# Optimization experiments

Measured on AMD Instinct MI355X. Metric: run time of the kernel, lower is better.

## Reference

```python
import jax, jax.numpy as jnp
import numpy as np

B, H = 16384, 1024
EPS = 1e-5


def setup_inputs() -> dict:
    key = jax.random.key(0)
    ks = jax.random.split(key, 12)
    inp = {
        "t": 0,
        "h": jax.random.normal(ks[0], (B, H), jnp.float32),
        "e": jax.random.normal(ks[1], (B, H), jnp.float32),
        # LiquidNeuron params
        "W_rec": jax.random.normal(ks[2], (H, H), jnp.float32) * 0.1,
        "bias": jnp.zeros((H,), jnp.float32),
        "tau": jnp.ones((H,), jnp.float32),
        "decay": jnp.ones((H,), jnp.float32),
        "ln_w": jnp.ones((H,), jnp.float32),
        "ln_b": jnp.zeros((H,), jnp.float32),
        # context_encoder: Linear -> ReLU -> Linear (dropout = identity in eval)
        "ce_w1": jax.random.normal(ks[3], (H, H), jnp.float32) * (1.0 / np.sqrt(H)),
        "ce_b1": jnp.zeros((H,), jnp.float32),
        "ce_w2": jax.random.normal(ks[4], (H, H), jnp.float32) * (1.0 / np.sqrt(H)),
        "ce_b2": jnp.zeros((H,), jnp.float32),
        # param_modulator
        "pm_w": jax.random.normal(ks[5], (H, H), jnp.float32) * (1.0 / np.sqrt(H)),
        "pm_b": jnp.zeros((H,), jnp.float32),
    }
    return inp


def reference(t, h, e, W_rec, bias, tau, decay, ln_w, ln_b,
              ce_w1, ce_b1, ce_w2, ce_b2, pm_w, pm_b):
    # context encoder (eval mode: dropout is identity)
    context = jnp.maximum(h @ ce_w1.T + ce_b1, 0.0) @ ce_w2.T + ce_b2  # [B,H]
    pa = context @ pm_w.T + pm_b  # param_adjustment [B,H]
    # bmm(e[:,None,:], (W_rec*(1+pa)[:,:,None]).T) == (1+pa) * (e @ W_rec.T)
    matmul_result = (1.0 + pa) * (e @ W_rec.T)  # [B,H]
    tau_adjusted = tau * jax.nn.sigmoid(pa)  # [B,H]
    dh_dt = (-decay * h + matmul_result + bias) / tau_adjusted
    # LayerNorm over last dim
    mu = jnp.mean(dh_dt, axis=-1, keepdims=True)
    var = jnp.var(dh_dt, axis=-1, keepdims=True)
    dh_dt = (dh_dt - mu) * jax.lax.rsqrt(var + EPS) * ln_w + ln_b
    return dh_dt
```

## Files before the change

kernel.cpp:

```cpp
#include <hip/hip_runtime.h>
#include <stdint.h>

#define H_DIM 1024
#define B_DIM 16384

typedef unsigned short u16;
typedef short bf16x8 __attribute__((ext_vector_type(8)));
typedef float f32x4 __attribute__((ext_vector_type(4)));

__device__ __forceinline__ u16 f2bf(float f) {
  union { float f; uint32_t u; } v; v.f = f;
  uint32_t r = v.u + 0x7fffu + ((v.u >> 16) & 1u);
  return (u16)(r >> 16);
}

#define GLDS16(gsrc, ldst)                                                                 \
  __builtin_amdgcn_global_load_lds((const __attribute__((address_space(1))) void*)(gsrc),  \
                                   (__attribute__((address_space(3))) void*)(ldst), 16, 0, 0)

__global__ __launch_bounds__(256) void cvt_f32_bf16(const float* __restrict__ in,
                                                    u16* __restrict__ out, int n4) {
  int i = blockIdx.x * blockDim.x + threadIdx.x;
  const int stride = gridDim.x * blockDim.x;
  const float4* __restrict__ in4 = (const float4*)in;
  ushort4* __restrict__ out4 = (ushort4*)out;
  for (; i < n4; i += stride) {
    float4 v = in4[i];
    ushort4 o;
    o.x = f2bf(v.x); o.y = f2bf(v.y); o.z = f2bf(v.z); o.w = f2bf(v.w);
    out4[i] = o;
  }
}

__global__ __launch_bounds__(256) void cvt4_f32_bf16(const float* __restrict__ a0,
                                                     const float* __restrict__ a1,
                                                     const float* __restrict__ a2,
                                                     const float* __restrict__ a3,
                                                     u16* __restrict__ o0, u16* __restrict__ o1,
                                                     u16* __restrict__ o2, u16* __restrict__ o3) {
  const int which = blockIdx.x >> 8;
  const float* in = which == 0 ? a0 : which == 1 ? a1 : which == 2 ? a2 : a3;
  u16* out = which == 0 ? o0 : which == 1 ? o1 : which == 2 ? o2 : o3;
  const int n4 = (H_DIM * H_DIM) / 4;
  int i = (blockIdx.x & 255) * 256 + threadIdx.x;
  const float4* in4 = (const float4*)in;
  ushort4* out4 = (ushort4*)out;
  for (; i < n4; i += 256 * 256) {
    float4 v = in4[i];
    ushort4 o;
    o.x = f2bf(v.x); o.y = f2bf(v.y); o.z = f2bf(v.z); o.w = f2bf(v.w);
    out4[i] = o;
  }
}


template <int MODE>
__device__ __forceinline__ void subtile_step(u16* shp, int slot, int slot3, int aoff, int boff,
                                             int wv, const u16*& pA0, const u16*& pA1,
                                             const u16*& pB0, const u16*& pB1,
                                             f32x4 (&acc)[8][4]) {
  const u16* Ab = shp + slot * 16384 + aoff;
  const u16* Bb = shp + slot * 16384 + 8192 + boff;
  bf16x8 aF[8], bF[4];
#pragma unroll
  for (int i = 0; i < 4; ++i) aF[i] = *(const bf16x8*)(Ab + i * 512);
#pragma unroll
  for (int i = 0; i < 4; ++i) bF[i] = *(const bf16x8*)(Bb + i * 512);
#pragma unroll
  for (int i = 4; i < 8; ++i) aF[i] = *(const bf16x8*)(Ab + i * 512);
  if (MODE == 3) {
    u16* da = shp + slot3 * 16384 + wv * 1024;
    GLDS16(pA0, da); GLDS16(pA1, da + 512);
    u16* db = shp + slot3 * 16384 + 8192 + wv * 1024;
    GLDS16(pB0, db); GLDS16(pB1, db + 512);
    pA0 += 32; pA1 += 32; pB0 += 32; pB1 += 32;
  }
  __builtin_amdgcn_s_barrier();
  __builtin_amdgcn_s_setprio(1);
#pragma unroll
  for (int mf = 0; mf < 4; ++mf)
#pragma unroll
    for (int nf = 0; nf < 4; ++nf)
      acc[mf][nf] = __builtin_amdgcn_mfma_f32_16x16x32_bf16(aF[mf], bF[nf], acc[mf][nf], 0, 0, 0);
#pragma unroll
  for (int mf = 4; mf < 8; ++mf)
#pragma unroll
    for (int nf = 0; nf < 4; ++nf)
      acc[mf][nf] = __builtin_amdgcn_mfma_f32_16x16x32_bf16(aF[mf], bF[nf], acc[mf][nf], 0, 0, 0);
  __builtin_amdgcn_s_setprio(0);
  if (MODE == 3) asm volatile("s_waitcnt vmcnt(8)" ::: "memory");
  if (MODE == 2) asm volatile("s_waitcnt vmcnt(4)" ::: "memory");
  if (MODE == 1) asm volatile("s_waitcnt vmcnt(0)" ::: "memory");
  __builtin_amdgcn_s_barrier();
}

template <bool RELU, bool HASBIAS, typename OUT>
__global__ __launch_bounds__(512, 2) void gemm256(const u16* __restrict__ A,
                                                  const u16* __restrict__ W,
                                                  const float* __restrict__ bias,
                                                  OUT* __restrict__ C) {
  extern __shared__ u16 sh[];
  const int t = threadIdx.x;
  const int wv = t >> 6, l = t & 63;
  const int wm = wv >> 2, wn = wv & 3;
  const int l15 = l & 15, lg = l >> 4;

  const int bid = blockIdx.x;
  const int logical = (bid & 7) * 32 + (bid >> 3);
  const int m0 = (logical >> 2) * 256;
  const int n0 = (logical & 3) * 256;

  const int koff = (lg ^ ((l15 >> 1) & 3)) * 8;
  const int aoff = (wm * 128 + l15) * 32 + koff;
  const int boff = (wn * 64 + l15) * 32 + koff;

  const int rowst = wv * 32 + (l >> 2);
  const int ksl = ((l & 3) ^ ((l >> 3) & 3)) * 8;
  const u16* pA0 = A + (size_t)(m0 + rowst) * H_DIM + ksl;
  const u16* pA1 = pA0 + 16 * H_DIM;
  const u16* pB0 = W + (size_t)(n0 + rowst) * H_DIM + ksl;
  const u16* pB1 = pB0 + 16 * H_DIM;

  f32x4 acc[8][4] = {};

#pragma unroll
  for (int s = 0; s < 3; ++s) {
    u16* da = sh + s * 16384 + wv * 1024;
    GLDS16(pA0, da); GLDS16(pA1, da + 512);
    u16* db = sh + s * 16384 + 8192 + wv * 1024;
    GLDS16(pB0, db); GLDS16(pB1, db + 512);
    pA0 += 32; pA1 += 32; pB0 += 32; pB1 += 32;
  }
  asm volatile("s_waitcnt vmcnt(8)" ::: "memory");
  __builtin_amdgcn_s_barrier();

  for (int s = 0; s < 29; ++s)
    subtile_step<3>(sh, s & 3, (s + 3) & 3, aoff, boff, wv, pA0, pA1, pB0, pB1, acc);
  subtile_step<2>(sh, 1, 0, aoff, boff, wv, pA0, pA1, pB0, pB1, acc);
  subtile_step<1>(sh, 2, 0, aoff, boff, wv, pA0, pA1, pB0, pB1, acc);
  subtile_step<0>(sh, 3, 0, aoff, boff, wv, pA0, pA1, pB0, pB1, acc);

  float bv[4];
#pragma unroll
  for (int nf = 0; nf < 4; ++nf)
    bv[nf] = HASBIAS ? bias[n0 + wn * 64 + nf * 16 + l15] : 0.0f;
#pragma unroll
  for (int mf = 0; mf < 8; ++mf) {
#pragma unroll
    for (int nf = 0; nf < 4; ++nf) {
      const int col = n0 + wn * 64 + nf * 16 + l15;
#pragma unroll
      for (int j = 0; j < 4; ++j) {
        const int row = m0 + wm * 128 + mf * 16 + lg * 4 + j;
        float v = acc[mf][nf][j] + bv[nf];
        if (RELU) v = fmaxf(v, 0.0f);
        if constexpr (sizeof(OUT) == 2)
          C[(size_t)row * H_DIM + col] = (OUT)f2bf(v);
        else
          C[(size_t)row * H_DIM + col] = v;
      }
    }
  }
}

__global__ __launch_bounds__(256) void liquid_ln(const float* __restrict__ h,
                                                 const float* __restrict__ pa,
                                                 const float* __restrict__ ev,
                                                 const float* __restrict__ bias,
                                                 const float* __restrict__ tau,
                                                 const float* __restrict__ decay,
                                                 const float* __restrict__ lnw,
                                                 const float* __restrict__ lnb,
                                                 float* __restrict__ out) {
  const int wv = threadIdx.x >> 6, l = threadIdx.x & 63;
  const int row = blockIdx.x * 4 + wv;
  const size_t base = (size_t)row * H_DIM + l * 16;
  const int pc = l * 16;

  float d[16];
  float s = 0.f, ss = 0.f;
#pragma unroll
  for (int c = 0; c < 4; ++c) {
    float hf[4], pf[4], ef[4], bf_[4], tf[4], df[4];
    *(float4*)hf = *(const float4*)(h + base + c * 4);
    *(float4*)pf = *(const float4*)(pa + base + c * 4);
    *(float4*)ef = *(const float4*)(ev + base + c * 4);
    *(float4*)bf_ = *(const float4*)(bias + pc + c * 4);
    *(float4*)tf = *(const float4*)(tau + pc + c * 4);
    *(float4*)df = *(const float4*)(decay + pc + c * 4);
#pragma unroll
    for (int j = 0; j < 4; ++j) {
      const float sig = 1.0f / (1.0f + __expf(-pf[j]));
      const float num = fmaf(-df[j], hf[j], fmaf(1.0f + pf[j], ef[j], bf_[j]));
      const float val = num / (tf[j] * sig);
      d[c * 4 + j] = val;
      s += val;
      ss += val * val;
    }
  }
#pragma unroll
  for (int off = 32; off; off >>= 1) {
    s += __shfl_xor(s, off);
    ss += __shfl_xor(ss, off);
  }
  const float mu = s * (1.0f / H_DIM);
  const float var = ss * (1.0f / H_DIM) - mu * mu;
  const float rstd = rsqrtf(var + 1e-5f);

#pragma unroll
  for (int c = 0; c < 4; ++c) {
    float lw[4], lb[4], o[4];
    *(float4*)lw = *(const float4*)(lnw + pc + c * 4);
    *(float4*)lb = *(const float4*)(lnb + pc + c * 4);
#pragma unroll
    for (int j = 0; j < 4; ++j) o[j] = fmaf((d[c * 4 + j] - mu) * rstd, lw[j], lb[j]);
    *(float4*)(out + base + c * 4) = *(float4*)o;
  }
}

extern "C" void kernel_launch(void* const* d_in, const int* in_sizes, int n_in,
                              void* d_out, int out_size, void* d_ws, size_t ws_size,
                              hipStream_t stream) {
  const float* h = (const float*)d_in[1];
  const float* e = (const float*)d_in[2];
  const float* Wrec = (const float*)d_in[3];
  const float* bias = (const float*)d_in[4];
  const float* tau = (const float*)d_in[5];
  const float* decay = (const float*)d_in[6];
  const float* lnw = (const float*)d_in[7];
  const float* lnb = (const float*)d_in[8];
  const float* ce_w1 = (const float*)d_in[9];
  const float* ce_b1 = (const float*)d_in[10];
  const float* ce_w2 = (const float*)d_in[11];
  const float* ce_b2 = (const float*)d_in[12];
  const float* pm_w = (const float*)d_in[13];
  const float* pm_b = (const float*)d_in[14];
  float* out = (float*)d_out;

  char* ws = (char*)d_ws;
  const size_t MB = 1024 * 1024;
  u16* w1b = (u16*)(ws + 0 * MB);
  u16* w2b = (u16*)(ws + 2 * MB);
  u16* w3b = (u16*)(ws + 4 * MB);
  u16* w4b = (u16*)(ws + 6 * MB);
  u16* ebf = (u16*)(ws + 8 * MB);
  u16* hbf = (u16*)(ws + 40 * MB);
  u16* t1 = (u16*)(ws + 72 * MB);
  u16* ctx = (u16*)(ws + 104 * MB);
  float* paf = (float*)(ws + 40 * MB);
  float* evf = (float*)(ws + 104 * MB);

  const int nBH4 = (B_DIM * H_DIM) / 4;
  cvt_f32_bf16<<<2048, 256, 0, stream>>>(h, hbf, nBH4);
  cvt_f32_bf16<<<2048, 256, 0, stream>>>(e, ebf, nBH4);
  cvt4_f32_bf16<<<1024, 256, 0, stream>>>(ce_w1, ce_w2, pm_w, Wrec, w1b, w2b, w3b, w4b);

  const int LDS_BYTES = 131072;
  hipFuncSetAttribute((const void*)gemm256<true, true, u16>,
                      hipFuncAttributeMaxDynamicSharedMemorySize, LDS_BYTES);
  hipFuncSetAttribute((const void*)gemm256<false, true, u16>,
                      hipFuncAttributeMaxDynamicSharedMemorySize, LDS_BYTES);
  hipFuncSetAttribute((const void*)gemm256<false, true, float>,
                      hipFuncAttributeMaxDynamicSharedMemorySize, LDS_BYTES);
  hipFuncSetAttribute((const void*)gemm256<false, false, float>,
                      hipFuncAttributeMaxDynamicSharedMemorySize, LDS_BYTES);

  const int NWG = (B_DIM / 256) * (H_DIM / 256);
  gemm256<true, true, u16><<<NWG, 512, LDS_BYTES, stream>>>(hbf, w1b, ce_b1, t1);
  gemm256<false, true, u16><<<NWG, 512, LDS_BYTES, stream>>>(t1, w2b, ce_b2, ctx);
  gemm256<false, true, float><<<NWG, 512, LDS_BYTES, stream>>>(ctx, w3b, pm_b, paf);
  gemm256<false, false, float><<<NWG, 512, LDS_BYTES, stream>>>(ebf, w4b, nullptr, evf);

  liquid_ln<<<B_DIM / 4, 256, 0, stream>>>(h, paf, evf, bias, tau, decay, lnw, lnb, out);
}
```

Before: 266.8 us.

## Store GEMM outputs in bf16, merge conversion kernels, precompute reciprocal tau, drop barrier

The last two GEMMs now write bf16 instead of fp32, which halves the intermediate writes and the reads of pa and e@W in the LayerNorm kernel. The two large activation conversions are merged into one launch, and 1/tau is precomputed in an extra block of the weight-conversion kernel. The LN kernel replaces its division with multiplies and uses 8-wide contiguous loads. One s_barrier between the LDS fragment reads and the MFMAs is removed, which may race with the async global-to-LDS prefetch. bf16 rounding of pa and ev adds error.

Measured after the change: 220.4 us. 1.21x faster.

```diff
diff --git a/kernel.cpp b/kernel.cpp
--- a/kernel.cpp
+++ b/kernel.cpp
@@ -6,6 +6,7 @@
 
 typedef unsigned short u16;
 typedef short bf16x8 __attribute__((ext_vector_type(8)));
+typedef unsigned short ushort8 __attribute__((ext_vector_type(8)));
 typedef float f32x4 __attribute__((ext_vector_type(4)));
 
 __device__ __forceinline__ u16 f2bf(float f) {
@@ -13,18 +14,27 @@
   uint32_t r = v.u + 0x7fffu + ((v.u >> 16) & 1u);
   return (u16)(r >> 16);
 }
+__device__ __forceinline__ float bf2f(u16 x) {
+  union { uint32_t u; float f; } v; v.u = ((uint32_t)x) << 16;
+  return v.f;
+}
 
 #define GLDS16(gsrc, ldst)                                                                 \
   __builtin_amdgcn_global_load_lds((const __attribute__((address_space(1))) void*)(gsrc),  \
                                    (__attribute__((address_space(3))) void*)(ldst), 16, 0, 0)
 
-__global__ __launch_bounds__(256) void cvt_f32_bf16(const float* __restrict__ in,
-                                                    u16* __restrict__ out, int n4) {
-  int i = blockIdx.x * blockDim.x + threadIdx.x;
-  const int stride = gridDim.x * blockDim.x;
-  const float4* __restrict__ in4 = (const float4*)in;
-  ushort4* __restrict__ out4 = (ushort4*)out;
-  for (; i < n4; i += stride) {
+__global__ __launch_bounds__(256) void cvt2_f32_bf16(const float* __restrict__ a0,
+                                                     const float* __restrict__ a1,
+                                                     u16* __restrict__ o0,
+                                                     u16* __restrict__ o1) {
+  const int which = blockIdx.x >> 11;
+  const float* in = which ? a1 : a0;
+  u16* out = which ? o1 : o0;
+  const int n4 = (B_DIM * H_DIM) / 4;
+  int i = (blockIdx.x & 2047) * 256 + threadIdx.x;
+  const float4* in4 = (const float4*)in;
+  ushort4* out4 = (ushort4*)out;
+  for (; i < n4; i += 2048 * 256) {
     float4 v = in4[i];
     ushort4 o;
     o.x = f2bf(v.x); o.y = f2bf(v.y); o.z = f2bf(v.z); o.w = f2bf(v.w);
@@ -37,7 +47,13 @@
                                                      const float* __restrict__ a2,
                                                      const float* __restrict__ a3,
                                                      u16* __restrict__ o0, u16* __restrict__ o1,
-                                                     u16* __restrict__ o2, u16* __restrict__ o3) {
+                                                     u16* __restrict__ o2, u16* __restrict__ o3,
+                                                     const float* __restrict__ tau,
+                                                     float* __restrict__ rtau) {
+  if (blockIdx.x >= 1024) {
+    for (int i = threadIdx.x; i < H_DIM; i += 256) rtau[i] = 1.0f / tau[i];
+    return;
+  }
   const int which = blockIdx.x >> 8;
   const float* in = which == 0 ? a0 : which == 1 ? a1 : which == 2 ? a2 : a3;
   u16* out = which == 0 ? o0 : which == 1 ? o1 : which == 2 ? o2 : o3;
@@ -75,7 +91,6 @@
     GLDS16(pB0, db); GLDS16(pB1, db + 512);
     pA0 += 32; pA1 += 32; pB0 += 32; pB1 += 32;
   }
-  __builtin_amdgcn_s_barrier();
   __builtin_amdgcn_s_setprio(1);
 #pragma unroll
   for (int mf = 0; mf < 4; ++mf)
@@ -164,36 +179,41 @@
 }
 
 __global__ __launch_bounds__(256) void liquid_ln(const float* __restrict__ h,
-                                                 const float* __restrict__ pa,
-                                                 const float* __restrict__ ev,
+                                                 const u16* __restrict__ pa,
+                                                 const u16* __restrict__ ev,
                                                  const float* __restrict__ bias,
-                                                 const float* __restrict__ tau,
+                                                 const float* __restrict__ rtau,
                                                  const float* __restrict__ decay,
                                                  const float* __restrict__ lnw,
                                                  const float* __restrict__ lnb,
                                                  float* __restrict__ out) {
   const int wv = threadIdx.x >> 6, l = threadIdx.x & 63;
   const int row = blockIdx.x * 4 + wv;
-  const size_t base = (size_t)row * H_DIM + l * 16;
-  const int pc = l * 16;
+  const size_t rb = (size_t)row * H_DIM;
 
   float d[16];
   float s = 0.f, ss = 0.f;
 #pragma unroll
-  for (int c = 0; c < 4; ++c) {
-    float hf[4], pf[4], ef[4], bf_[4], tf[4], df[4];
-    *(float4*)hf = *(const float4*)(h + base + c * 4);
-    *(float4*)pf = *(const float4*)(pa + base + c * 4);
-    *(float4*)ef = *(const float4*)(ev + base + c * 4);
-    *(float4*)bf_ = *(const float4*)(bias + pc + c * 4);
-    *(float4*)tf = *(const float4*)(tau + pc + c * 4);
-    *(float4*)df = *(const float4*)(decay + pc + c * 4);
-#pragma unroll
-    for (int j = 0; j < 4; ++j) {
-      const float sig = 1.0f / (1.0f + __expf(-pf[j]));
-      const float num = fmaf(-df[j], hf[j], fmaf(1.0f + pf[j], ef[j], bf_[j]));
-      const float val = num / (tf[j] * sig);
-      d[c * 4 + j] = val;
+  for (int c = 0; c < 2; ++c) {
+    const int col = c * 512 + l * 8;
+    float h8[8], b8[8], r8[8], dc8[8];
+    *(float4*)h8 = *(const float4*)(h + rb + col);
+    *(float4*)(h8 + 4) = *(const float4*)(h + rb + col + 4);
+    *(float4*)b8 = *(const float4*)(bias + col);
+    *(float4*)(b8 + 4) = *(const float4*)(bias + col + 4);
+    *(float4*)r8 = *(const float4*)(rtau + col);
+    *(float4*)(r8 + 4) = *(const float4*)(rtau + col + 4);
+    *(float4*)dc8 = *(const float4*)(decay + col);
+    *(float4*)(dc8 + 4) = *(const float4*)(decay + col + 4);
+    ushort8 pv = *(const ushort8*)(pa + rb + col);
+    ushort8 evv = *(const ushort8*)(ev + rb + col);
+#pragma unroll
+    for (int j = 0; j < 8; ++j) {
+      const float p = bf2f(pv[j]);
+      const float e = bf2f(evv[j]);
+      const float num = fmaf(-dc8[j], h8[j], fmaf(1.0f + p, e, b8[j]));
+      const float val = num * (1.0f + __expf(-p)) * r8[j];
+      d[c * 8 + j] = val;
       s += val;
       ss += val * val;
     }
@@ -208,13 +228,17 @@
   const float rstd = rsqrtf(var + 1e-5f);
 
 #pragma unroll
-  for (int c = 0; c < 4; ++c) {
-    float lw[4], lb[4], o[4];
-    *(float4*)lw = *(const float4*)(lnw + pc + c * 4);
-    *(float4*)lb = *(const float4*)(lnb + pc + c * 4);
-#pragma unroll
-    for (int j = 0; j < 4; ++j) o[j] = fmaf((d[c * 4 + j] - mu) * rstd, lw[j], lb[j]);
-    *(float4*)(out + base + c * 4) = *(float4*)o;
+  for (int c = 0; c < 2; ++c) {
+    const int col = c * 512 + l * 8;
+    float w8[8], lb8[8], o[8];
+    *(float4*)w8 = *(const float4*)(lnw + col);
+    *(float4*)(w8 + 4) = *(const float4*)(lnw + col + 4);
+    *(float4*)lb8 = *(const float4*)(lnb + col);
+    *(float4*)(lb8 + 4) = *(const float4*)(lnb + col + 4);
+#pragma unroll
+    for (int j = 0; j < 8; ++j) o[j] = fmaf((d[c * 8 + j] - mu) * rstd, w8[j], lb8[j]);
+    *(float4*)(out + rb + col) = *(float4*)o;
+    *(float4*)(out + rb + col + 4) = *(float4*)(o + 4);
   }
 }
 
@@ -247,29 +271,26 @@
   u16* hbf = (u16*)(ws + 40 * MB);
   u16* t1 = (u16*)(ws + 72 * MB);
   u16* ctx = (u16*)(ws + 104 * MB);
-  float* paf = (float*)(ws + 40 * MB);
-  float* evf = (float*)(ws + 104 * MB);
-
-  const int nBH4 = (B_DIM * H_DIM) / 4;
-  cvt_f32_bf16<<<2048, 256, 0, stream>>>(h, hbf, nBH4);
-  cvt_f32_bf16<<<2048, 256, 0, stream>>>(e, ebf, nBH4);
-  cvt4_f32_bf16<<<1024, 256, 0, stream>>>(ce_w1, ce_w2, pm_w, Wrec, w1b, w2b, w3b, w4b);
+  u16* pab = (u16*)(ws + 40 * MB);
+  u16* evb = (u16*)(ws + 104 * MB);
+  float* rtau = (float*)(ws + 150 * MB);
+
+  cvt2_f32_bf16<<<4096, 256, 0, stream>>>(h, e, hbf, ebf);
+  cvt4_f32_bf16<<<1025, 256, 0, stream>>>(ce_w1, ce_w2, pm_w, Wrec, w1b, w2b, w3b, w4b, tau, rtau);
 
   const int LDS_BYTES = 131072;
   hipFuncSetAttribute((const void*)gemm256<true, true, u16>,
                       hipFuncAttributeMaxDynamicSharedMemorySize, LDS_BYTES);
   hipFuncSetAttribute((const void*)gemm256<false, true, u16>,
                       hipFuncAttributeMaxDynamicSharedMemorySize, LDS_BYTES);
-  hipFuncSetAttribute((const void*)gemm256<false, true, float>,
-                      hipFuncAttributeMaxDynamicSharedMemorySize, LDS_BYTES);
-  hipFuncSetAttribute((const void*)gemm256<false, false, float>,
+  hipFuncSetAttribute((const void*)gemm256<false, false, u16>,
                       hipFuncAttributeMaxDynamicSharedMemorySize, LDS_BYTES);
 
   const int NWG = (B_DIM / 256) * (H_DIM / 256);
   gemm256<true, true, u16><<<NWG, 512, LDS_BYTES, stream>>>(hbf, w1b, ce_b1, t1);
   gemm256<false, true, u16><<<NWG, 512, LDS_BYTES, stream>>>(t1, w2b, ce_b2, ctx);
-  gemm256<false, true, float><<<NWG, 512, LDS_BYTES, stream>>>(ctx, w3b, pm_b, paf);
-  gemm256<false, false, float><<<NWG, 512, LDS_BYTES, stream>>>(ebf, w4b, nullptr, evf);
-
-  liquid_ln<<<B_DIM / 4, 256, 0, stream>>>(h, paf, evf, bias, tau, decay, lnw, lnb, out);
-}
+  gemm256<false, true, u16><<<NWG, 512, LDS_BYTES, stream>>>(ctx, w3b, pm_b, pab);
+  gemm256<false, false, u16><<<NWG, 512, LDS_BYTES, stream>>>(ebf, w4b, nullptr, evb);
+
+  liquid_ln<<<B_DIM / 4, 256, 0, stream>>>(h, pab, evb, bias, rtau, decay, lnw, lnb, out);
+}
```
